# Kernel optimization log

Measured on AMD Instinct MI355X. Metric: run time of the kernel, lower is better.

Reference implementation:

```python
import jax, jax.numpy as jnp
import numpy as np

B, Q, KV = 8, 16, 2048
NQ, NK, NV, H = 512, 512, 512, 512

def setup_inputs() -> dict:
    key = jax.random.key(0)
    k = jax.random.split(key, 7)
    s = 0.02
    return {
        "query": jax.random.normal(k[0], (B, Q, NQ), jnp.float32),
        "keys": jax.random.normal(k[1], (B, KV, NK), jnp.float32),
        "values": jax.random.normal(k[2], (B, KV, NV), jnp.float32),
        "W_weight": jax.random.normal(k[3], (H, NQ + NK), jnp.float32) * s,
        "W_bias": jax.random.normal(k[4], (H,), jnp.float32) * s,
        "v_weight": jax.random.normal(k[5], (1, H), jnp.float32) * s,
        "v_bias": jax.random.normal(k[6], (1,), jnp.float32) * s,
    }

def reference(query, keys, values, W_weight, W_bias, v_weight, v_bias):
    # Split W over the concat axis: cat([query, keys]) @ W^T == query@Wq^T + keys@Wk^T
    Wq = W_weight[:, :NQ]   # [H, Nq]
    Wk = W_weight[:, NQ:]   # [H, Nk]
    q_part = jnp.einsum('bqn,hn->bqh', query, Wq)   # [B,Q,H]
    k_part = jnp.einsum('bkn,hn->bkh', keys, Wk)    # [B,KV,H]
    # broadcast-add -> [B,KV,Q,H], tanh, project to scalar energy
    energy = jnp.tanh(k_part[:, :, None, :] + q_part[:, None, :, :] + W_bias)
    e = jnp.einsum('bkqh,h->bkq', energy, v_weight[0]) + v_bias[0]  # [B,KV,Q]
    scores = jax.nn.softmax(e, axis=1)              # softmax over KV
    # output = (values^T @ scores)^T -> [B,Q,Nv]
    output = jnp.einsum('bkn,bkq->bqn', values, scores)
    return output
```

## Files before the change

### kernel.cpp

```cpp
#include <hip/hip_runtime.h>
#include <cstddef>

using bf16x8  = __attribute__((ext_vector_type(8))) short;
using short4v = __attribute__((ext_vector_type(4))) short;
using f32x4   = __attribute__((ext_vector_type(4))) float;
using ushort8 = __attribute__((ext_vector_type(8))) unsigned short;

#define GLL16(gp, lp) __builtin_amdgcn_global_load_lds( \
    (const __attribute__((address_space(1))) unsigned int*)(const void*)(gp), \
    (__attribute__((address_space(3))) unsigned int*)(void*)(lp), 16, 0, 0)

__device__ __forceinline__ float exp2_f(float x){ float r; asm("v_exp_f32 %0, %1" : "=v"(r) : "v"(x)); return r; }
__device__ __forceinline__ float rcp_f (float x){ float r; asm("v_rcp_f32 %0, %1" : "=v"(r) : "v"(x)); return r; }
__device__ __forceinline__ unsigned short f2bf(float f){
  unsigned int u = __float_as_uint(f);
  u = u + 0x7FFFu + ((u >> 16) & 1u);
  return (unsigned short)(u >> 16);
}
__device__ __forceinline__ float bf2f(unsigned short s){
  return __uint_as_float(((unsigned int)s) << 16);
}

#define KEYS_N   8388608
#define SCALE_2LOG2E 2.885390081777927f

#define OFF_KEYS_BF   0u
#define OFF_WK_BF     16777216u
#define OFF_EQB       17301504u
#define OFF_EPART     17563648u
#define OFF_SC        21757952u

__global__ __launch_bounds__(256) void k_convert(
    const float* __restrict__ keys, const float* __restrict__ W,
    unsigned short* __restrict__ keys_bf, unsigned short* __restrict__ wk_bf)
{
  int idx = (blockIdx.x * 256 + threadIdx.x) * 8;
  const float* src;
  unsigned short* dst;
  if (idx < KEYS_N) { src = keys + idx; dst = keys_bf + idx; }
  else {
    int e = idx - KEYS_N;
    src = W + (size_t)(e >> 9) * 1024 + 512 + (e & 511);
    dst = wk_bf + e;
  }
  float4 a = *(const float4*)src;
  float4 b = *(const float4*)(src + 4);
  ushort8 o;
  o[0]=f2bf(a.x); o[1]=f2bf(a.y); o[2]=f2bf(a.z); o[3]=f2bf(a.w);
  o[4]=f2bf(b.x); o[5]=f2bf(b.y); o[6]=f2bf(b.z); o[7]=f2bf(b.w);
  *(ushort8*)dst = o;
}

__global__ __launch_bounds__(256) void k_convq(
    const float* __restrict__ query, const float* __restrict__ W,
    unsigned short* __restrict__ qw_bf)
{
  int idx = (blockIdx.x * 256 + threadIdx.x) * 8;
  const float* src;
  if (idx < 65536) src = query + idx;
  else { int e = idx - 65536; src = W + (size_t)(e >> 9) * 1024 + (e & 511); }
  float4 a = *(const float4*)src;
  float4 b = *(const float4*)(src + 4);
  ushort8 o;
  o[0]=f2bf(a.x); o[1]=f2bf(a.y); o[2]=f2bf(a.z); o[3]=f2bf(a.w);
  o[4]=f2bf(b.x); o[5]=f2bf(b.y); o[6]=f2bf(b.z); o[7]=f2bf(b.w);
  *(ushort8*)&qw_bf[idx] = o;
}

__global__ __launch_bounds__(256) void k_qgemm(
    const unsigned short* __restrict__ query_bf, float* __restrict__ eqb)
{
  __shared__ struct { short A[128*64]; short B[32*64]; } g;
  const int tid = threadIdx.x;
  const int l = tid & 63, w = tid >> 6;
  const int n0 = blockIdx.x * 32;
  const int wm = w & 1, wn = w >> 1;
  const int fr = l & 15, fg = l >> 4;
  const int axk = fr & 7;

  f32x4 acc[4];
  #pragma unroll
  for (int i = 0; i < 4; ++i) acc[i] = (f32x4){0.f,0.f,0.f,0.f};

  const int srow8 = (l >> 3);
  const int schk  = ((l & 7) ^ srow8) * 8;

  for (int kt = 0; kt < 8; ++kt) {
    const int k0 = kt * 64;
    #pragma unroll
    for (int r = 0; r < 4; ++r)
      GLL16(query_bf + (size_t)(r * 32 + w * 8 + srow8) * 512 + k0 + schk,
            &g.A[r * 2048 + w * 512]);
    GLL16(query_bf + (size_t)(128 + n0 + w * 8 + srow8) * 512 + k0 + schk,
          &g.B[w * 512]);
    __syncthreads();
    #pragma unroll
    for (int ks = 0; ks < 2; ++ks) {
      bf16x8 af[4], bfv;
      #pragma unroll
      for (int i = 0; i < 4; ++i)
        af[i] = *(const bf16x8*)&g.A[(wm*64 + i*16 + fr) * 64 + ((ks*4 + fg) ^ axk) * 8];
      bfv = *(const bf16x8*)&g.B[(wn*16 + fr) * 64 + ((ks*4 + fg) ^ axk) * 8];
      #pragma unroll
      for (int i = 0; i < 4; ++i)
        acc[i] = __builtin_amdgcn_mfma_f32_16x16x32_bf16(af[i], bfv, acc[i], 0, 0, 0);
    }
    __syncthreads();
  }
  const int gh = n0 + wn*16 + fr;
  #pragma unroll
  for (int i = 0; i < 4; ++i)
    #pragma unroll
    for (int r = 0; r < 4; ++r) {
      const int gm = wm*64 + i*16 + fg*4 + r;
      eqb[gm * 512 + gh] = exp2_f(acc[i][r] * SCALE_2LOG2E);
    }
}

struct FusedSM {
  union {
    struct { short A[8192]; short B[8192]; } g;
    unsigned short ekbf[128 * 128];
  } u;
  float eqs[16 * 128];
};

__global__ __launch_bounds__(256, 3) void k_fused(
    const unsigned short* __restrict__ keys_bf, const unsigned short* __restrict__ wk_bf,
    const float* __restrict__ w_bias, const float* __restrict__ eqb,
    const float* __restrict__ vw, float* __restrict__ e_part)
{
  __shared__ FusedSM sm;
  const int tid = threadIdx.x;
  const int l = tid & 63, w = tid >> 6;
  const int by = blockIdx.x;
  const int hc = blockIdx.y;
  const int h0 = hc * 128;
  const int b  = by >> 4;

  {
    const int q = tid >> 4, c0 = (tid & 15) * 8;
    const float* src = eqb + (size_t)(b * 16 + q) * 512 + h0 + c0;
    *(float4*)&sm.eqs[q * 128 + c0]     = *(const float4*)src;
    *(float4*)&sm.eqs[q * 128 + c0 + 4] = *(const float4*)(src + 4);
  }

  const unsigned short* Aptr = keys_bf + (size_t)by * 128 * 512;
  const unsigned short* Bptr = wk_bf + (size_t)h0 * 512;

  const int srow = w * 32 + (l >> 3);
  const int scol = ((l & 7) ^ (l >> 3)) * 8;
  const int wm = w >> 1, wn = w & 1;
  const int fr = l & 15, fg = l >> 4;
  const int axk = fr & 7;

  f32x4 acc[4][4];
  #pragma unroll
  for (int i = 0; i < 4; ++i)
    #pragma unroll
    for (int j = 0; j < 4; ++j) acc[i][j] = (f32x4){0.f,0.f,0.f,0.f};

  for (int kt = 0; kt < 8; ++kt) {
    const int k0 = kt * 64;
    #pragma unroll
    for (int r = 0; r < 4; ++r) {
      GLL16(Aptr + (srow + r * 8) * 512 + k0 + scol, &sm.u.g.A[w * 2048 + r * 512]);
      GLL16(Bptr + (srow + r * 8) * 512 + k0 + scol, &sm.u.g.B[w * 2048 + r * 512]);
    }
    __syncthreads();
    #pragma unroll
    for (int ks = 0; ks < 2; ++ks) {
      bf16x8 af[4], bfv[4];
      #pragma unroll
      for (int i = 0; i < 4; ++i) {
        af[i]  = *(const bf16x8*)&sm.u.g.A[(wm*64 + i*16 + fr) * 64 + ((ks*4 + fg) ^ axk) * 8];
        bfv[i] = *(const bf16x8*)&sm.u.g.B[(wn*64 + i*16 + fr) * 64 + ((ks*4 + fg) ^ axk) * 8];
      }
      #pragma unroll
      for (int i = 0; i < 4; ++i)
        #pragma unroll
        for (int j = 0; j < 4; ++j)
          acc[i][j] = __builtin_amdgcn_mfma_f32_16x16x32_bf16(af[i], bfv[j], acc[i][j], 0, 0, 0);
    }
    __syncthreads();
  }

  #pragma unroll
  for (int j = 0; j < 4; ++j) {
    const int col = wn*64 + j*16 + fr;
    const float bias = w_bias[h0 + col];
    const int chunk = col >> 3, coff = col & 7;
    #pragma unroll
    for (int i = 0; i < 4; ++i)
      #pragma unroll
      for (int r = 0; r < 4; ++r) {
        const int row = wm*64 + i*16 + fg*4 + r;
        const float ev = exp2_f((acc[i][j][r] + bias) * SCALE_2LOG2E);
        sm.u.ekbf[row * 128 + ((chunk ^ (fg*4 + r)) << 3) + coff] = f2bf(ev);
      }
  }
  const int g = l & 3, kl = l >> 2;
  float vv[32];
  #pragma unroll
  for (int s = 0; s < 4; ++s) {
    const float4 a0 = *(const float4*)(vw + h0 + s*32 + g*4);
    const float4 a1 = *(const float4*)(vw + h0 + s*32 + 16 + g*4);
    vv[s*8+0]=-2.f*a0.x; vv[s*8+1]=-2.f*a0.y; vv[s*8+2]=-2.f*a0.z; vv[s*8+3]=-2.f*a0.w;
    vv[s*8+4]=-2.f*a1.x; vv[s*8+5]=-2.f*a1.y; vv[s*8+6]=-2.f*a1.z; vv[s*8+7]=-2.f*a1.w;
  }
  __syncthreads();

  #pragma unroll
  for (int p = 0; p < 2; ++p) {
    const int lr = w * 32 + p * 16 + kl;
    float ek[32];
    #pragma unroll
    for (int s = 0; s < 4; ++s)
      #pragma unroll
      for (int hf = 0; hf < 2; ++hf) {
        const int ck = (4*s + 2*hf + (g >> 1)) ^ kl;
        const short4v v4 = *(const short4v*)&sm.u.ekbf[lr * 128 + (ck << 3) + (g & 1) * 4];
        ek[s*8 + hf*4 + 0] = bf2f((unsigned short)v4[0]);
        ek[s*8 + hf*4 + 1] = bf2f((unsigned short)v4[1]);
        ek[s*8 + hf*4 + 2] = bf2f((unsigned short)v4[2]);
        ek[s*8 + hf*4 + 3] = bf2f((unsigned short)v4[3]);
      }
    const size_t epbase = (size_t)hc * 262144 + ((size_t)(by * 128 + lr)) * 16;
    #pragma unroll 2
    for (int q = 0; q < 16; ++q) {
      float a0 = 0.f, a1 = 0.f;
      #pragma unroll
      for (int s = 0; s < 4; ++s) {
        const float* er = &sm.eqs[q * 128 + s * 32 + g * 4];
        const float4 E0 = *(const float4*)er;
        const float4 E1 = *(const float4*)(er + 16);
        a0 = fmaf(vv[s*8+0], rcp_f(fmaf(ek[s*8+0], E0.x, 1.f)), a0);
        a1 = fmaf(vv[s*8+1], rcp_f(fmaf(ek[s*8+1], E0.y, 1.f)), a1);
        a0 = fmaf(vv[s*8+2], rcp_f(fmaf(ek[s*8+2], E0.z, 1.f)), a0);
        a1 = fmaf(vv[s*8+3], rcp_f(fmaf(ek[s*8+3], E0.w, 1.f)), a1);
        a0 = fmaf(vv[s*8+4], rcp_f(fmaf(ek[s*8+4], E1.x, 1.f)), a0);
        a1 = fmaf(vv[s*8+5], rcp_f(fmaf(ek[s*8+5], E1.y, 1.f)), a1);
        a0 = fmaf(vv[s*8+6], rcp_f(fmaf(ek[s*8+6], E1.z, 1.f)), a0);
        a1 = fmaf(vv[s*8+7], rcp_f(fmaf(ek[s*8+7], E1.w, 1.f)), a1);
      }
      float a = a0 + a1;
      a += __shfl_xor(a, 1, 64);
      a += __shfl_xor(a, 2, 64);
      if (g == 0) e_part[epbase + q] = a;
    }
  }
}

__global__ __launch_bounds__(256) void k_softmax(
    const float* __restrict__ e_part, float* __restrict__ sc)
{
  const int b = blockIdx.x >> 4, q = blockIdx.x & 15;
  const int base = b * 32768 + q;
  const int tid = threadIdx.x;
  __shared__ float redm[4], reds[4];

  float vals[8];
  float mx = -1e30f;
  #pragma unroll
  for (int i = 0; i < 8; ++i) {
    const int x = base + (tid + i * 256) * 16;
    vals[i] = (e_part[x] + e_part[x + 262144]) + (e_part[x + 524288] + e_part[x + 786432]);
    mx = fmaxf(mx, vals[i]);
  }
  #pragma unroll
  for (int msk = 1; msk < 64; msk <<= 1) mx = fmaxf(mx, __shfl_xor(mx, msk, 64));
  if ((tid & 63) == 0) redm[tid >> 6] = mx;
  __syncthreads();
  mx = fmaxf(fmaxf(redm[0], redm[1]), fmaxf(redm[2], redm[3]));

  float ex[8], sum = 0.f;
  #pragma unroll
  for (int i = 0; i < 8; ++i) { ex[i] = __expf(vals[i] - mx); sum += ex[i]; }
  #pragma unroll
  for (int msk = 1; msk < 64; msk <<= 1) sum += __shfl_xor(sum, msk, 64);
  if ((tid & 63) == 0) reds[tid >> 6] = sum;
  __syncthreads();
  sum = reds[0] + reds[1] + reds[2] + reds[3];
  const float r = 1.f / sum;
  #pragma unroll
  for (int i = 0; i < 8; ++i) sc[base + (tid + i * 256) * 16] = ex[i] * r;
}

__global__ __launch_bounds__(256) void k_pv(
    const float* __restrict__ values, const float* __restrict__ sc,
    float* __restrict__ out)
{
  __shared__ float lds[2048];
  const int tid = threadIdx.x;
  const int nc = blockIdx.x & 31, b = blockIdx.x >> 5;
  const int n = tid & 15, kg = tid >> 4;
  const int l = tid & 63, w = tid >> 6;
  const int n0 = nc * 16;

  float acc[16];
  #pragma unroll
  for (int q = 0; q < 16; ++q) acc[q] = 0.f;

  for (int kc = 0; kc < 16; ++kc) {
    __syncthreads();
    const float* ssrc = sc + (size_t)(b * 2048 + kc * 128) * 16;
    *(float4*)&lds[tid * 8]     = *(const float4*)&ssrc[tid * 8];
    *(float4*)&lds[tid * 8 + 4] = *(const float4*)&ssrc[tid * 8 + 4];
    __syncthreads();
    const float* vb = values + ((size_t)(b * 2048 + kc * 128 + kg * 8)) * 512 + n0 + n;
    #pragma unroll
    for (int k2 = 0; k2 < 8; ++k2) {
      const float v = vb[(size_t)k2 * 512];
      const float* sr = &lds[(kg * 8 + k2) * 16];
      #pragma unroll
      for (int qq = 0; qq < 4; ++qq) {
        const float4 s4 = *(const float4*)&sr[qq * 4];
        acc[qq*4+0] = fmaf(v, s4.x, acc[qq*4+0]);
        acc[qq*4+1] = fmaf(v, s4.y, acc[qq*4+1]);
        acc[qq*4+2] = fmaf(v, s4.z, acc[qq*4+2]);
        acc[qq*4+3] = fmaf(v, s4.w, acc[qq*4+3]);
      }
    }
  }
  #pragma unroll
  for (int q = 0; q < 16; ++q) {
    acc[q] += __shfl_xor(acc[q], 16, 64);
    acc[q] += __shfl_xor(acc[q], 32, 64);
  }
  __syncthreads();
  if (l < 16) {
    #pragma unroll
    for (int q = 0; q < 16; ++q) lds[w * 256 + q * 16 + l] = acc[q];
  }
  __syncthreads();
  const int q = tid >> 4, nn = tid & 15;
  const float s = (lds[q * 16 + nn] + lds[256 + q * 16 + nn]) +
                  (lds[512 + q * 16 + nn] + lds[768 + q * 16 + nn]);
  out[((size_t)(b * 16 + q)) * 512 + n0 + nn] = s;
}

extern "C" void kernel_launch(void* const* d_in, const int* in_sizes, int n_in,
                              void* d_out, int out_size, void* d_ws, size_t ws_size,
                              hipStream_t stream)
{
  const float* query  = (const float*)d_in[0];
  const float* keys   = (const float*)d_in[1];
  const float* values = (const float*)d_in[2];
  const float* W      = (const float*)d_in[3];
  const float* w_bias = (const float*)d_in[4];
  const float* vw     = (const float*)d_in[5];

  char* ws = (char*)d_ws;
  unsigned short* keys_bf = (unsigned short*)(ws + OFF_KEYS_BF);
  unsigned short* wk_bf   = (unsigned short*)(ws + OFF_WK_BF);
  float* eqb    = (float*)(ws + OFF_EQB);
  float* e_part = (float*)(ws + OFF_EPART);
  float* sc     = (float*)(ws + OFF_SC);
  unsigned short* qw_bf = (unsigned short*)(ws + OFF_EPART);

  hipLaunchKernelGGL(k_convq, dim3(160), dim3(256), 0, stream, query, W, qw_bf);
  hipLaunchKernelGGL(k_convert, dim3(4224), dim3(256), 0, stream,
                     keys, W, keys_bf, wk_bf);
  hipLaunchKernelGGL(k_qgemm, dim3(16), dim3(256), 0, stream, qw_bf, eqb);
  hipLaunchKernelGGL(k_fused, dim3(128, 4), dim3(256), 0, stream,
                     keys_bf, wk_bf, w_bias, eqb, vw, e_part);
  hipLaunchKernelGGL(k_softmax, dim3(128), dim3(256), 0, stream, e_part, sc);
  hipLaunchKernelGGL(k_pv, dim3(256), dim3(256), 0, stream, values, sc, (float*)d_out);
}
```

Before: 93.97 us.

## Fold query GEMM into convert kernel, interleave energy rows, widen PV blocks

The separate query-conversion and query-GEMM kernels are removed. Their work now runs as 16 extra blocks of the keys-conversion kernel, which convert fp32 to bf16 in registers with a packed convert instruction before the MFMA. This drops two launches and the intermediate bf16 buffer. The fused energy kernel now processes two rows per thread in one loop, giving more independent rcp/fma chains for ILP at the cost of more registers. The PV kernel moves to 512 threads with a padded LDS layout and an 8-way final reduction.

After: 87.52 us. -6.9%, faster.

```diff
diff --git a/kernel.cpp b/kernel.cpp
--- a/kernel.cpp
+++ b/kernel.cpp
@@ -12,6 +12,9 @@
 
 __device__ __forceinline__ float exp2_f(float x){ float r; asm("v_exp_f32 %0, %1" : "=v"(r) : "v"(x)); return r; }
 __device__ __forceinline__ float rcp_f (float x){ float r; asm("v_rcp_f32 %0, %1" : "=v"(r) : "v"(x)); return r; }
+__device__ __forceinline__ unsigned pk2(float lo, float hi){
+  unsigned r; asm("v_cvt_pk_bf16_f32 %0, %1, %2" : "=v"(r) : "v"(lo), "v"(hi)); return r;
+}
 __device__ __forceinline__ unsigned short f2bf(float f){
   unsigned int u = __float_as_uint(f);
   u = u + 0x7FFFu + ((u >> 16) & 1u);
@@ -22,6 +25,8 @@
 }
 
 #define KEYS_N   8388608
+#define WK_N     262144
+#define CONV_BLOCKS 4224
 #define SCALE_2LOG2E 2.885390081777927f
 
 #define OFF_KEYS_BF   0u
@@ -32,8 +37,68 @@
 
 __global__ __launch_bounds__(256) void k_convert(
     const float* __restrict__ keys, const float* __restrict__ W,
-    unsigned short* __restrict__ keys_bf, unsigned short* __restrict__ wk_bf)
-{
+    const float* __restrict__ query,
+    unsigned short* __restrict__ keys_bf, unsigned short* __restrict__ wk_bf,
+    float* __restrict__ eqb)
+{
+  __shared__ short qg[128*32 + 32*32];
+  if (blockIdx.x >= CONV_BLOCKS) {
+    const int nb = blockIdx.x - CONV_BLOCKS;
+    const int n0 = nb * 32;
+    const int tid = threadIdx.x;
+    const int l = tid & 63, w = tid >> 6;
+    short* A  = qg;
+    short* Bs = qg + 4096;
+    const int sub = tid >> 3;
+    const int c4  = (tid & 7) * 4;
+    const int wm = w & 1, wn = w >> 1;
+    const int fr = l & 15, fg = l >> 4;
+
+    f32x4 acc[4];
+    #pragma unroll
+    for (int i = 0; i < 4; ++i) acc[i] = (f32x4){0.f,0.f,0.f,0.f};
+
+    for (int kt = 0; kt < 16; ++kt) {
+      const int k0 = kt * 32;
+      float4 a4[4];
+      #pragma unroll
+      for (int m = 0; m < 4; ++m)
+        a4[m] = *(const float4*)(query + (size_t)(m * 32 + sub) * 512 + k0 + c4);
+      const float4 b4 = *(const float4*)(W + (size_t)(n0 + sub) * 1024 + k0 + c4);
+      __syncthreads();
+      #pragma unroll
+      for (int m = 0; m < 4; ++m) {
+        const int row = m * 32 + sub;
+        const int o = row * 32 + (((c4 >> 3) ^ ((row >> 1) & 3)) << 3) + (c4 & 7);
+        *(uint2*)&A[o] = make_uint2(pk2(a4[m].x, a4[m].y), pk2(a4[m].z, a4[m].w));
+      }
+      {
+        const int o = sub * 32 + (((c4 >> 3) ^ ((sub >> 1) & 3)) << 3) + (c4 & 7);
+        *(uint2*)&Bs[o] = make_uint2(pk2(b4.x, b4.y), pk2(b4.z, b4.w));
+      }
+      __syncthreads();
+      bf16x8 af[4], bfv;
+      #pragma unroll
+      for (int i = 0; i < 4; ++i) {
+        const int ar = wm*64 + i*16 + fr;
+        af[i] = *(const bf16x8*)&A[ar*32 + ((fg ^ ((ar>>1)&3)) << 3)];
+      }
+      const int br = wn*16 + fr;
+      bfv = *(const bf16x8*)&Bs[br*32 + ((fg ^ ((br>>1)&3)) << 3)];
+      #pragma unroll
+      for (int i = 0; i < 4; ++i)
+        acc[i] = __builtin_amdgcn_mfma_f32_16x16x32_bf16(af[i], bfv, acc[i], 0, 0, 0);
+    }
+    const int gh = n0 + wn*16 + fr;
+    #pragma unroll
+    for (int i = 0; i < 4; ++i)
+      #pragma unroll
+      for (int r = 0; r < 4; ++r) {
+        const int gm = wm*64 + i*16 + fg*4 + r;
+        eqb[gm * 512 + gh] = exp2_f(acc[i][r] * SCALE_2LOG2E);
+      }
+    return;
+  }
   int idx = (blockIdx.x * 256 + threadIdx.x) * 8;
   const float* src;
   unsigned short* dst;
@@ -51,72 +116,6 @@
   *(ushort8*)dst = o;
 }
 
-__global__ __launch_bounds__(256) void k_convq(
-    const float* __restrict__ query, const float* __restrict__ W,
-    unsigned short* __restrict__ qw_bf)
-{
-  int idx = (blockIdx.x * 256 + threadIdx.x) * 8;
-  const float* src;
-  if (idx < 65536) src = query + idx;
-  else { int e = idx - 65536; src = W + (size_t)(e >> 9) * 1024 + (e & 511); }
-  float4 a = *(const float4*)src;
-  float4 b = *(const float4*)(src + 4);
-  ushort8 o;
-  o[0]=f2bf(a.x); o[1]=f2bf(a.y); o[2]=f2bf(a.z); o[3]=f2bf(a.w);
-  o[4]=f2bf(b.x); o[5]=f2bf(b.y); o[6]=f2bf(b.z); o[7]=f2bf(b.w);
-  *(ushort8*)&qw_bf[idx] = o;
-}
-
-__global__ __launch_bounds__(256) void k_qgemm(
-    const unsigned short* __restrict__ query_bf, float* __restrict__ eqb)
-{
-  __shared__ struct { short A[128*64]; short B[32*64]; } g;
-  const int tid = threadIdx.x;
-  const int l = tid & 63, w = tid >> 6;
-  const int n0 = blockIdx.x * 32;
-  const int wm = w & 1, wn = w >> 1;
-  const int fr = l & 15, fg = l >> 4;
-  const int axk = fr & 7;
-
-  f32x4 acc[4];
-  #pragma unroll
-  for (int i = 0; i < 4; ++i) acc[i] = (f32x4){0.f,0.f,0.f,0.f};
-
-  const int srow8 = (l >> 3);
-  const int schk  = ((l & 7) ^ srow8) * 8;
-
-  for (int kt = 0; kt < 8; ++kt) {
-    const int k0 = kt * 64;
-    #pragma unroll
-    for (int r = 0; r < 4; ++r)
-      GLL16(query_bf + (size_t)(r * 32 + w * 8 + srow8) * 512 + k0 + schk,
-            &g.A[r * 2048 + w * 512]);
-    GLL16(query_bf + (size_t)(128 + n0 + w * 8 + srow8) * 512 + k0 + schk,
-          &g.B[w * 512]);
-    __syncthreads();
-    #pragma unroll
-    for (int ks = 0; ks < 2; ++ks) {
-      bf16x8 af[4], bfv;
-      #pragma unroll
-      for (int i = 0; i < 4; ++i)
-        af[i] = *(const bf16x8*)&g.A[(wm*64 + i*16 + fr) * 64 + ((ks*4 + fg) ^ axk) * 8];
-      bfv = *(const bf16x8*)&g.B[(wn*16 + fr) * 64 + ((ks*4 + fg) ^ axk) * 8];
-      #pragma unroll
-      for (int i = 0; i < 4; ++i)
-        acc[i] = __builtin_amdgcn_mfma_f32_16x16x32_bf16(af[i], bfv, acc[i], 0, 0, 0);
-    }
-    __syncthreads();
-  }
-  const int gh = n0 + wn*16 + fr;
-  #pragma unroll
-  for (int i = 0; i < 4; ++i)
-    #pragma unroll
-    for (int r = 0; r < 4; ++r) {
-      const int gm = wm*64 + i*16 + fg*4 + r;
-      eqb[gm * 512 + gh] = exp2_f(acc[i][r] * SCALE_2LOG2E);
-    }
-}
-
 struct FusedSM {
   union {
     struct { short A[8192]; short B[8192]; } g;
@@ -210,43 +209,57 @@
   }
   __syncthreads();
 
-  #pragma unroll
-  for (int p = 0; p < 2; ++p) {
-    const int lr = w * 32 + p * 16 + kl;
-    float ek[32];
+  {
+    const int lr0 = w * 32 + kl;
+    const int lr1 = lr0 + 16;
+    float ek0[32], ek1[32];
     #pragma unroll
     for (int s = 0; s < 4; ++s)
       #pragma unroll
       for (int hf = 0; hf < 2; ++hf) {
         const int ck = (4*s + 2*hf + (g >> 1)) ^ kl;
-        const short4v v4 = *(const short4v*)&sm.u.ekbf[lr * 128 + (ck << 3) + (g & 1) * 4];
-        ek[s*8 + hf*4 + 0] = bf2f((unsigned short)v4[0]);
-        ek[s*8 + hf*4 + 1] = bf2f((unsigned short)v4[1]);
-        ek[s*8 + hf*4 + 2] = bf2f((unsigned short)v4[2]);
-        ek[s*8 + hf*4 + 3] = bf2f((unsigned short)v4[3]);
-      }
-    const size_t epbase = (size_t)hc * 262144 + ((size_t)(by * 128 + lr)) * 16;
+        const short4v v40 = *(const short4v*)&sm.u.ekbf[lr0 * 128 + (ck << 3) + (g & 1) * 4];
+        const short4v v41 = *(const short4v*)&sm.u.ekbf[lr1 * 128 + (ck << 3) + (g & 1) * 4];
+        #pragma unroll
+        for (int u = 0; u < 4; ++u) {
+          ek0[s*8 + hf*4 + u] = bf2f((unsigned short)v40[u]);
+          ek1[s*8 + hf*4 + u] = bf2f((unsigned short)v41[u]);
+        }
+      }
+    const size_t ep0 = (size_t)hc * 262144 + ((size_t)(by * 128 + lr0)) * 16;
+    const size_t ep1 = (size_t)hc * 262144 + ((size_t)(by * 128 + lr1)) * 16;
     #pragma unroll 2
     for (int q = 0; q < 16; ++q) {
-      float a0 = 0.f, a1 = 0.f;
+      float a00 = 0.f, a01 = 0.f, a10 = 0.f, a11 = 0.f;
       #pragma unroll
       for (int s = 0; s < 4; ++s) {
         const float* er = &sm.eqs[q * 128 + s * 32 + g * 4];
         const float4 E0 = *(const float4*)er;
         const float4 E1 = *(const float4*)(er + 16);
-        a0 = fmaf(vv[s*8+0], rcp_f(fmaf(ek[s*8+0], E0.x, 1.f)), a0);
-        a1 = fmaf(vv[s*8+1], rcp_f(fmaf(ek[s*8+1], E0.y, 1.f)), a1);
-        a0 = fmaf(vv[s*8+2], rcp_f(fmaf(ek[s*8+2], E0.z, 1.f)), a0);
-        a1 = fmaf(vv[s*8+3], rcp_f(fmaf(ek[s*8+3], E0.w, 1.f)), a1);
-        a0 = fmaf(vv[s*8+4], rcp_f(fmaf(ek[s*8+4], E1.x, 1.f)), a0);
-        a1 = fmaf(vv[s*8+5], rcp_f(fmaf(ek[s*8+5], E1.y, 1.f)), a1);
-        a0 = fmaf(vv[s*8+6], rcp_f(fmaf(ek[s*8+6], E1.z, 1.f)), a0);
-        a1 = fmaf(vv[s*8+7], rcp_f(fmaf(ek[s*8+7], E1.w, 1.f)), a1);
-      }
-      float a = a0 + a1;
-      a += __shfl_xor(a, 1, 64);
-      a += __shfl_xor(a, 2, 64);
-      if (g == 0) e_part[epbase + q] = a;
+        a00 = fmaf(vv[s*8+0], rcp_f(fmaf(ek0[s*8+0], E0.x, 1.f)), a00);
+        a01 = fmaf(vv[s*8+1], rcp_f(fmaf(ek0[s*8+1], E0.y, 1.f)), a01);
+        a00 = fmaf(vv[s*8+2], rcp_f(fmaf(ek0[s*8+2], E0.z, 1.f)), a00);
+        a01 = fmaf(vv[s*8+3], rcp_f(fmaf(ek0[s*8+3], E0.w, 1.f)), a01);
+        a00 = fmaf(vv[s*8+4], rcp_f(fmaf(ek0[s*8+4], E1.x, 1.f)), a00);
+        a01 = fmaf(vv[s*8+5], rcp_f(fmaf(ek0[s*8+5], E1.y, 1.f)), a01);
+        a00 = fmaf(vv[s*8+6], rcp_f(fmaf(ek0[s*8+6], E1.z, 1.f)), a00);
+        a01 = fmaf(vv[s*8+7], rcp_f(fmaf(ek0[s*8+7], E1.w, 1.f)), a01);
+        a10 = fmaf(vv[s*8+0], rcp_f(fmaf(ek1[s*8+0], E0.x, 1.f)), a10);
+        a11 = fmaf(vv[s*8+1], rcp_f(fmaf(ek1[s*8+1], E0.y, 1.f)), a11);
+        a10 = fmaf(vv[s*8+2], rcp_f(fmaf(ek1[s*8+2], E0.z, 1.f)), a10);
+        a11 = fmaf(vv[s*8+3], rcp_f(fmaf(ek1[s*8+3], E0.w, 1.f)), a11);
+        a10 = fmaf(vv[s*8+4], rcp_f(fmaf(ek1[s*8+4], E1.x, 1.f)), a10);
+        a11 = fmaf(vv[s*8+5], rcp_f(fmaf(ek1[s*8+5], E1.y, 1.f)), a11);
+        a10 = fmaf(vv[s*8+6], rcp_f(fmaf(ek1[s*8+6], E1.z, 1.f)), a10);
+        a11 = fmaf(vv[s*8+7], rcp_f(fmaf(ek1[s*8+7], E1.w, 1.f)), a11);
+      }
+      float r0 = a00 + a01;
+      r0 += __shfl_xor(r0, 1, 64);
+      r0 += __shfl_xor(r0, 2, 64);
+      float r1 = a10 + a11;
+      r1 += __shfl_xor(r1, 1, 64);
+      r1 += __shfl_xor(r1, 2, 64);
+      if (g == 0) { e_part[ep0 + q] = r0; e_part[ep1 + q] = r1; }
     }
   }
 }
@@ -286,11 +299,11 @@
   for (int i = 0; i < 8; ++i) sc[base + (tid + i * 256) * 16] = ex[i] * r;
 }
 
-__global__ __launch_bounds__(256) void k_pv(
+__global__ __launch_bounds__(512) void k_pv(
     const float* __restrict__ values, const float* __restrict__ sc,
     float* __restrict__ out)
 {
-  __shared__ float lds[2048];
+  __shared__ float lds[128 * 20];
   const int tid = threadIdx.x;
   const int nc = blockIdx.x & 31, b = blockIdx.x >> 5;
   const int n = tid & 15, kg = tid >> 4;
@@ -303,15 +316,17 @@
 
   for (int kc = 0; kc < 16; ++kc) {
     __syncthreads();
-    const float* ssrc = sc + (size_t)(b * 2048 + kc * 128) * 16;
-    *(float4*)&lds[tid * 8]     = *(const float4*)&ssrc[tid * 8];
-    *(float4*)&lds[tid * 8 + 4] = *(const float4*)&ssrc[tid * 8 + 4];
+    {
+      const float* ssrc = sc + (size_t)(b * 2048 + kc * 128) * 16;
+      const int row = tid >> 2, c4 = (tid & 3) * 4;
+      *(float4*)&lds[row * 20 + c4] = *(const float4*)&ssrc[row * 16 + c4];
+    }
     __syncthreads();
-    const float* vb = values + ((size_t)(b * 2048 + kc * 128 + kg * 8)) * 512 + n0 + n;
-    #pragma unroll
-    for (int k2 = 0; k2 < 8; ++k2) {
+    const float* vb = values + ((size_t)(b * 2048 + kc * 128 + kg * 4)) * 512 + n0 + n;
+    #pragma unroll
+    for (int k2 = 0; k2 < 4; ++k2) {
       const float v = vb[(size_t)k2 * 512];
-      const float* sr = &lds[(kg * 8 + k2) * 16];
+      const float* sr = &lds[(kg * 4 + k2) * 20];
       #pragma unroll
       for (int qq = 0; qq < 4; ++qq) {
         const float4 s4 = *(const float4*)&sr[qq * 4];
@@ -333,10 +348,13 @@
     for (int q = 0; q < 16; ++q) lds[w * 256 + q * 16 + l] = acc[q];
   }
   __syncthreads();
-  const int q = tid >> 4, nn = tid & 15;
-  const float s = (lds[q * 16 + nn] + lds[256 + q * 16 + nn]) +
-                  (lds[512 + q * 16 + nn] + lds[768 + q * 16 + nn]);
-  out[((size_t)(b * 16 + q)) * 512 + n0 + nn] = s;
+  if (tid < 256) {
+    const int q = tid >> 4, nn = tid & 15;
+    float s = 0.f;
+    #pragma unroll
+    for (int w2 = 0; w2 < 8; ++w2) s += lds[w2 * 256 + q * 16 + nn];
+    out[((size_t)(b * 16 + q)) * 512 + n0 + nn] = s;
+  }
 }
 
 extern "C" void kernel_launch(void* const* d_in, const int* in_sizes, int n_in,
@@ -356,14 +374,11 @@
   float* eqb    = (float*)(ws + OFF_EQB);
   float* e_part = (float*)(ws + OFF_EPART);
   float* sc     = (float*)(ws + OFF_SC);
-  unsigned short* qw_bf = (unsigned short*)(ws + OFF_EPART);
-
-  hipLaunchKernelGGL(k_convq, dim3(160), dim3(256), 0, stream, query, W, qw_bf);
-  hipLaunchKernelGGL(k_convert, dim3(4224), dim3(256), 0, stream,
-                     keys, W, keys_bf, wk_bf);
-  hipLaunchKernelGGL(k_qgemm, dim3(16), dim3(256), 0, stream, qw_bf, eqb);
+
+  hipLaunchKernelGGL(k_convert, dim3(CONV_BLOCKS + 16), dim3(256), 0, stream,
+                     keys, W, query, keys_bf, wk_bf, eqb);
   hipLaunchKernelGGL(k_fused, dim3(128, 4), dim3(256), 0, stream,
                      keys_bf, wk_bf, w_bias, eqb, vw, e_part);
   hipLaunchKernelGGL(k_softmax, dim3(128), dim3(256), 0, stream, e_part, sc);
-  hipLaunchKernelGGL(k_pv, dim3(256), dim3(256), 0, stream, values, sc, (float*)d_out);
-}
+  hipLaunchKernelGGL(k_pv, dim3(256), dim3(512), 0, stream, values, sc, (float*)d_out);
+}
```
